# Kernel optimization log

Hardware: AMD Instinct MI355X
Metric: run time of the kernel (lower is better)

## Reference

```python
import jax, jax.numpy as jnp
import numpy as np

NUM_NODES = 10000


def setup_inputs() -> dict:
    key = jax.random.key(0)
    k1, k2, k3, k4 = jax.random.split(key, 4)
    x = jax.random.normal(k1, (NUM_NODES, 128), dtype=jnp.float32)
    edge_index = jax.random.randint(k2, (2, 640000), 0, NUM_NODES, dtype=jnp.int64)
    W = jax.random.normal(k3, (128, 128), dtype=jnp.float32) * (1.0 / np.sqrt(128))
    b = jax.random.normal(k4, (128,), dtype=jnp.float32) * 0.01
    return {"x": x, "edge_index": edge_index, "W": W, "b": b}


def reference(x, edge_index, W, b):
    src, dst = edge_index[0], edge_index[1]
    num_nodes = x.shape[0]
    # scatter-add: aggregated[dst] += x[src]
    aggregated = jax.ops.segment_sum(x[src], dst, num_segments=num_nodes)
    # in-degree normalization (clamped at 1)
    degree = jax.ops.segment_sum(jnp.ones_like(dst, dtype=x.dtype), dst,
                                 num_segments=num_nodes)
    degree = jnp.maximum(degree, 1.0)
    aggregated = aggregated / degree[:, None]
    # linear (y = h @ W.T + b) + ReLU
    out = jax.nn.relu(jnp.einsum('nd,od->no', aggregated + x, W) + b)
    return out
```

## Files before the change

### kernel.cpp

```cpp
#include <hip/hip_runtime.h>
#include <hip/hip_bf16.h>
#include <hip/hip_fp8.h>
#include <hip/hip_cooperative_groups.h>

namespace cg = cooperative_groups;

#define NB    64
#define EPB   10000
#define NPAD  10240
#define NPT   40
#define NGEMM 625
#define LCAP  1024
#define GRID_FUSED (NGEMM + NB)
#define SMEM_BYTES 40496

typedef __bf16 bf16_8 __attribute__((ext_vector_type(8)));
typedef float f32_2 __attribute__((ext_vector_type(2)));
typedef float f32_4 __attribute__((ext_vector_type(4)));
typedef float f32_8 __attribute__((ext_vector_type(8)));

__device__ __forceinline__ void gemm_role(unsigned char* smem, int bx,
    const float* __restrict__ x, const float* __restrict__ W,
    __hip_bfloat16* __restrict__ zb, unsigned char* __restrict__ zb8) {
  float* ctile = (float*)smem;
  const int rowbase = bx * 16;
  const int wid = threadIdx.x >> 6;
  const int lane = threadIdx.x & 63;
  const int m16 = lane & 15;
  const int quad = lane >> 4;

  union { bf16_8 v; __hip_bfloat16 h8[8]; } ac[4];
  const float* arow = x + (size_t)(rowbase + m16) * 128 + quad * 8;
#pragma unroll
  for (int kk = 0; kk < 4; ++kk) {
    f32_8 af = *(const f32_8*)(arow + kk * 32);
#pragma unroll
    for (int j = 0; j < 8; ++j) ac[kk].h8[j] = __float2bfloat16(af[j]);
  }
#pragma unroll
  for (int ct = 0; ct < 2; ++ct) {
    int colbase = wid * 32 + ct * 16;
    const float* brow = W + (size_t)(colbase + m16) * 128 + quad * 8;
    f32_4 c = {0.f, 0.f, 0.f, 0.f};
#pragma unroll
    for (int kk = 0; kk < 4; ++kk) {
      f32_8 bf = *(const f32_8*)(brow + kk * 32);
      union { bf16_8 v; __hip_bfloat16 h8[8]; } bc;
#pragma unroll
      for (int j = 0; j < 8; ++j) bc.h8[j] = __float2bfloat16(bf[j]);
      c = __builtin_amdgcn_mfma_f32_16x16x32_bf16(ac[kk].v, bc.v, c, 0, 0, 0);
    }
#pragma unroll
    for (int r = 0; r < 4; ++r)
      ctile[(quad * 4 + r) * 132 + colbase + m16] = c[r];
  }
  __syncthreads();

  const int row = threadIdx.x >> 4;
  const int cs = (threadIdx.x & 15) * 8;
  const float* src = ctile + row * 132 + cs;
  f32_4 a0 = *(const f32_4*)(src);
  f32_4 a1 = *(const f32_4*)(src + 4);
  union { uint4 u; __hip_bfloat16 h[8]; } hb;
  union { uint2 u; unsigned char c[8]; } q8;
#pragma unroll
  for (int j = 0; j < 4; ++j) {
    hb.h[j] = __float2bfloat16(a0[j]);
    hb.h[4 + j] = __float2bfloat16(a1[j]);
    q8.c[j] = __hip_fp8_e4m3(a0[j]).__x;
    q8.c[4 + j] = __hip_fp8_e4m3(a1[j]).__x;
  }
  *(uint4*)(zb + (size_t)(rowbase + row) * 128 + cs) = hb.u;
  *(uint2*)(zb8 + (size_t)(rowbase + row) * 128 + cs) = q8.u;
}

__device__ __forceinline__ void sort_role(unsigned char* smem, int b,
    const int* __restrict__ ei, int E,
    unsigned short* __restrict__ bins, unsigned int* __restrict__ combo) {
  int* h = (int*)smem;
  unsigned short* sorted = (unsigned short*)(smem + 20480);
  int* wsum = (int*)(smem + 40480);

  const int t = threadIdx.x;
  const int4* src4 = (const int4*)(ei) + b * (EPB / 4);
  const int4* dst4 = (const int4*)(ei + E) + b * (EPB / 4);

  for (int i = t; i < NPAD / 2; i += 256) h[i] = 0;
  __syncthreads();

  for (int i = t; i < EPB / 4; i += 256) {
    int4 d = dst4[i];
    atomicAdd(&h[d.x >> 1], 1 << ((d.x & 1) * 16));
    atomicAdd(&h[d.y >> 1], 1 << ((d.y & 1) * 16));
    atomicAdd(&h[d.z >> 1], 1 << ((d.z & 1) * 16));
    atomicAdd(&h[d.w >> 1], 1 << ((d.w & 1) * 16));
  }
  __syncthreads();

  int raw[NPT];
  const int lo = t * NPT;
  int sum = 0;
#pragma unroll
  for (int j = 0; j < NPT; j += 2) {
    int pair = h[(lo + j) >> 1];
    raw[j] = pair & 0xFFFF;
    raw[j + 1] = (pair >> 16) & 0xFFFF;
    sum += raw[j] + raw[j + 1];
  }
  int incl = sum;
#pragma unroll
  for (int off = 1; off < 64; off <<= 1) {
    int v = __shfl_up(incl, off);
    if ((t & 63) >= off) incl += v;
  }
  if ((t & 63) == 63) wsum[t >> 6] = incl;
  __syncthreads();
  int wb = 0;
  for (int w = 0; w < (t >> 6); ++w) wb += wsum[w];
  int run = wb + incl - sum;

  unsigned int cpack[NPT];
#pragma unroll
  for (int j = 0; j < NPT; j += 2) {
    int r0 = run; run += raw[j];
    int r1 = run; run += raw[j + 1];
    h[(lo + j) >> 1] = (r1 << 16) | r0;
    cpack[j]     = ((unsigned)raw[j] << 16) | (unsigned)r0;
    cpack[j + 1] = ((unsigned)raw[j + 1] << 16) | (unsigned)r1;
  }
  __syncthreads();

  unsigned int* crow = combo + (size_t)b * NPAD + lo;
#pragma unroll
  for (int j = 0; j < NPT; j += 4)
    *(uint4*)(crow + j) = make_uint4(cpack[j], cpack[j+1], cpack[j+2], cpack[j+3]);

  for (int i = t; i < EPB / 4; i += 256) {
    int4 s4 = src4[i];
    int4 d4 = dst4[i];
    int ss[4] = {s4.x, s4.y, s4.z, s4.w};
    int dd[4] = {d4.x, d4.y, d4.z, d4.w};
#pragma unroll
    for (int u = 0; u < 4; ++u) {
      int nn = dd[u];
      int sh = (nn & 1) * 16;
      int pos = (atomicAdd(&h[nn >> 1], 1 << sh) >> sh) & 0xFFFF;
      sorted[pos] = (unsigned short)ss[u];
    }
  }
  __syncthreads();

  unsigned int* outb = (unsigned int*)(bins + (size_t)b * EPB);
  const unsigned int* s32 = (const unsigned int*)sorted;
  for (int i = t; i < EPB / 2; i += 256) outb[i] = s32[i];
}

__device__ __forceinline__ void agg_quad(unsigned char* smem, int q,
    const unsigned int* __restrict__ combo, const unsigned short* __restrict__ bins,
    const unsigned char* __restrict__ zb8, const __hip_bfloat16* __restrict__ zb,
    const float* __restrict__ bias, float* __restrict__ out, int N) {
  unsigned int* trans = (unsigned int*)smem;
  unsigned short* list = (unsigned short*)(smem + 1024);
  int* cursor = (int*)(smem + 9216);

  const int t = threadIdx.x;
  const int wid = t >> 6;
  const int lane = t & 63;
  const int n0 = q * 4;

  __syncthreads();
  if (t < 4) cursor[t] = 0;
  if (t < 64) {
    uint4 cm = *(const uint4*)(combo + (size_t)t * NPAD + n0);
    trans[t] = cm.x; trans[64 + t] = cm.y; trans[128 + t] = cm.z; trans[192 + t] = cm.w;
  }
  __syncthreads();

  const int n = n0 + wid;
  unsigned int cc = trans[wid * 64 + lane];
  int c = (int)(cc >> 16);
  int o = (int)(cc & 0xFFFF);

  int p = atomicAdd(&cursor[wid], c);

  {
    const unsigned short* bk = bins + (size_t)lane * EPB + o;
    unsigned short* L = list + wid * LCAP;
    unsigned short s0 = 0, s1 = 0, s2 = 0;
    if (c > 0) s0 = bk[0];
    if (c > 1) s1 = bk[1];
    if (c > 2) s2 = bk[2];
    if (c > 0 && p < LCAP) L[p] = s0;
    if (c > 1 && p + 1 < LCAP) L[p + 1] = s1;
    if (c > 2 && p + 2 < LCAP) L[p + 2] = s2;
    for (int j = 3; j < c; ++j)
      if (p + j < LCAP) L[p + j] = bk[j];
  }
  __syncthreads();

  const int m = cursor[wid];
  const int g = lane >> 3;
  const int sub = lane & 7;
  int mm = m < LCAP ? m : LCAP;
  const unsigned short* L = list + wid * LCAP;
  const unsigned char* z8base = zb8 + sub * 16;

  float acc[16];
#pragma unroll
  for (int k = 0; k < 16; ++k) acc[k] = 0.f;

  for (int e = 0; e < mm; e += 64) {
    uint4 v[8];
#pragma unroll
    for (int u = 0; u < 8; ++u) {
      int idx = e + u * 8 + g;
      v[u] = make_uint4(0u, 0u, 0u, 0u);
      if (idx < mm) {
        int s = L[idx];
        v[u] = *(const uint4*)(z8base + (size_t)s * 128);
      }
    }
#pragma unroll
    for (int u = 0; u < 8; ++u) {
      f32_2 p01 = __builtin_amdgcn_cvt_pk_f32_fp8((int)v[u].x, false);
      f32_2 p23 = __builtin_amdgcn_cvt_pk_f32_fp8((int)v[u].x, true);
      f32_2 p45 = __builtin_amdgcn_cvt_pk_f32_fp8((int)v[u].y, false);
      f32_2 p67 = __builtin_amdgcn_cvt_pk_f32_fp8((int)v[u].y, true);
      f32_2 p89 = __builtin_amdgcn_cvt_pk_f32_fp8((int)v[u].z, false);
      f32_2 pab = __builtin_amdgcn_cvt_pk_f32_fp8((int)v[u].z, true);
      f32_2 pcd = __builtin_amdgcn_cvt_pk_f32_fp8((int)v[u].w, false);
      f32_2 pef = __builtin_amdgcn_cvt_pk_f32_fp8((int)v[u].w, true);
      acc[0] += p01[0];  acc[1] += p01[1];  acc[2] += p23[0];  acc[3] += p23[1];
      acc[4] += p45[0];  acc[5] += p45[1];  acc[6] += p67[0];  acc[7] += p67[1];
      acc[8] += p89[0];  acc[9] += p89[1];  acc[10] += pab[0]; acc[11] += pab[1];
      acc[12] += pcd[0]; acc[13] += pcd[1]; acc[14] += pef[0]; acc[15] += pef[1];
    }
  }
#pragma unroll
  for (int k = 0; k < 16; ++k) {
    acc[k] += __shfl_xor(acc[k], 8);
    acc[k] += __shfl_xor(acc[k], 16);
    acc[k] += __shfl_xor(acc[k], 32);
  }

  if (g == 0 && n < N) {
    float inv = 1.f / (float)(m > 0 ? m : 1);
    const __hip_bfloat16* znp = zb + (size_t)n * 128 + sub * 16;
    bf16_8 z0 = *(const bf16_8*)znp;
    bf16_8 z1 = *(const bf16_8*)(znp + 8);
    const float* bp = bias + sub * 16;
    f32_8 b0 = *(const f32_8*)bp;
    f32_8 b1 = *(const f32_8*)(bp + 8);
    float r[16];
#pragma unroll
    for (int k = 0; k < 8; ++k) {
      float v2 = acc[k] * inv + (float)z0[k] + b0[k];
      r[k] = v2 > 0.f ? v2 : 0.f;
    }
#pragma unroll
    for (int k = 0; k < 8; ++k) {
      float v2 = acc[8 + k] * inv + (float)z1[k] + b1[k];
      r[8 + k] = v2 > 0.f ? v2 : 0.f;
    }
    float* o2 = out + (size_t)n * 128 + sub * 16;
    *(float4*)(o2)      = make_float4(r[0], r[1], r[2], r[3]);
    *(float4*)(o2 + 4)  = make_float4(r[4], r[5], r[6], r[7]);
    *(float4*)(o2 + 8)  = make_float4(r[8], r[9], r[10], r[11]);
    *(float4*)(o2 + 12) = make_float4(r[12], r[13], r[14], r[15]);
  }
}

__global__ void __launch_bounds__(256, 3) k_all(
    const float* __restrict__ x, const int* __restrict__ ei,
    const float* __restrict__ W, const float* __restrict__ bias,
    __hip_bfloat16* __restrict__ zb, unsigned char* __restrict__ zb8,
    unsigned short* __restrict__ bins, unsigned int* __restrict__ combo,
    float* __restrict__ out, int E, int N) {
  __shared__ __align__(16) unsigned char smem[SMEM_BYTES];
  if (blockIdx.x < NGEMM) gemm_role(smem, blockIdx.x, x, W, zb, zb8);
  else sort_role(smem, blockIdx.x - NGEMM, ei, E, bins, combo);
  __threadfence();
  cg::this_grid().sync();
  const int NQ = N >> 2;
  for (int q = blockIdx.x; q < NQ; q += gridDim.x)
    agg_quad(smem, q, combo, bins, zb8, zb, bias, out, N);
}

__global__ void __launch_bounds__(256, 3) k_phase1(
    const float* __restrict__ x, const int* __restrict__ ei,
    const float* __restrict__ W,
    __hip_bfloat16* __restrict__ zb, unsigned char* __restrict__ zb8,
    unsigned short* __restrict__ bins, unsigned int* __restrict__ combo, int E) {
  __shared__ __align__(16) unsigned char smem[SMEM_BYTES];
  if (blockIdx.x < NGEMM) gemm_role(smem, blockIdx.x, x, W, zb, zb8);
  else sort_role(smem, blockIdx.x - NGEMM, ei, E, bins, combo);
}

__global__ void __launch_bounds__(256) k_phase2(
    const unsigned int* __restrict__ combo, const unsigned short* __restrict__ bins,
    const unsigned char* __restrict__ zb8, const __hip_bfloat16* __restrict__ zb,
    const float* __restrict__ bias, float* __restrict__ out, int N) {
  __shared__ __align__(16) unsigned char smem[9232];
  agg_quad(smem, blockIdx.x, combo, bins, zb8, zb, bias, out, N);
}

extern "C" void kernel_launch(void* const* d_in, const int* in_sizes, int n_in,
                              void* d_out, int out_size, void* d_ws, size_t ws_size,
                              hipStream_t stream) {
  const float* x = (const float*)d_in[0];
  const int* ei = (const int*)d_in[1];
  const float* W = (const float*)d_in[2];
  const float* b = (const float*)d_in[3];
  float* out = (float*)d_out;

  const int N = in_sizes[0] / 128;
  const int E = in_sizes[1] / 2;

  char* ws = (char*)d_ws;
  size_t off = 0;
  auto carve = [&](size_t bytes) {
    void* p = ws + off;
    off = (off + bytes + 255) & ~(size_t)255;
    return p;
  };
  __hip_bfloat16* zb = (__hip_bfloat16*)carve((size_t)N * 128 * 2);
  unsigned char* zb8 = (unsigned char*)carve((size_t)N * 128);
  unsigned short* bins = (unsigned short*)carve((size_t)NB * EPB * 2);
  unsigned int* combo = (unsigned int*)carve((size_t)NB * NPAD * 4);

  static int coop = -1;
  bool done = false;
  if (coop != 0) {
    bool try_now = true;
    if (coop == -1) {
      hipStreamCaptureStatus st = hipStreamCaptureStatusNone;
      (void)hipStreamIsCapturing(stream, &st);
      if (st != hipStreamCaptureStatusNone) try_now = false;
    }
    if (try_now) {
      void* args[] = {(void*)&x, (void*)&ei, (void*)&W, (void*)&b,
                      (void*)&zb, (void*)&zb8, (void*)&bins, (void*)&combo,
                      (void*)&out, (void*)&E, (void*)&N};
      hipError_t err = hipLaunchCooperativeKernel((const void*)k_all, dim3(GRID_FUSED),
                                                  dim3(256), args, 0, stream);
      if (err == hipSuccess) {
        coop = 1;
        done = true;
      } else {
        coop = 0;
        (void)hipGetLastError();
      }
    }
  }
  if (!done) {
    k_phase1<<<GRID_FUSED, 256, 0, stream>>>(x, ei, W, zb, zb8, bins, combo, E);
    k_phase2<<<N / 4, 256, 0, stream>>>(combo, bins, zb8, zb, b, out, N);
  }
}
```

Baseline: 101.0 us.

## Replace cooperative grid-sync kernel with two launches and wave-scan list building

Drops the cooperative single-kernel path with a grid-wide barrier and always launches a phase-1 kernel followed by a separate aggregation kernel with 2500 blocks and higher occupancy bounds. The aggregation kernel replaces the shared-memory atomic cursor with a wavefront shuffle prefix scan, which removes a block barrier. The sort role's edge loops are manually unrolled to issue two int4 loads per iteration for more memory parallelism. The cost is an extra kernel launch boundary in exchange for avoiding grid-sync overhead and the persistent-loop imbalance.

```diff
diff --git a/kernel.cpp b/kernel.cpp
--- a/kernel.cpp
+++ b/kernel.cpp
@@ -1,9 +1,6 @@
 #include <hip/hip_runtime.h>
 #include <hip/hip_bf16.h>
 #include <hip/hip_fp8.h>
-#include <hip/hip_cooperative_groups.h>
-
-namespace cg = cooperative_groups;
 
 #define NB    64
 #define EPB   10000
@@ -11,7 +8,6 @@
 #define NPT   40
 #define NGEMM 625
 #define LCAP  1024
-#define GRID_FUSED (NGEMM + NB)
 #define SMEM_BYTES 40496
 
 typedef __bf16 bf16_8 __attribute__((ext_vector_type(8)));
@@ -88,8 +84,29 @@
   for (int i = t; i < NPAD / 2; i += 256) h[i] = 0;
   __syncthreads();
 
-  for (int i = t; i < EPB / 4; i += 256) {
-    int4 d = dst4[i];
+#pragma unroll
+  for (int k = 0; k < 4; ++k) {
+    int i0 = t + k * 512;
+    int4 d0 = dst4[i0];
+    int4 d1 = dst4[i0 + 256];
+    atomicAdd(&h[d0.x >> 1], 1 << ((d0.x & 1) * 16));
+    atomicAdd(&h[d0.y >> 1], 1 << ((d0.y & 1) * 16));
+    atomicAdd(&h[d0.z >> 1], 1 << ((d0.z & 1) * 16));
+    atomicAdd(&h[d0.w >> 1], 1 << ((d0.w & 1) * 16));
+    atomicAdd(&h[d1.x >> 1], 1 << ((d1.x & 1) * 16));
+    atomicAdd(&h[d1.y >> 1], 1 << ((d1.y & 1) * 16));
+    atomicAdd(&h[d1.z >> 1], 1 << ((d1.z & 1) * 16));
+    atomicAdd(&h[d1.w >> 1], 1 << ((d1.w & 1) * 16));
+  }
+  {
+    int4 d = dst4[2048 + t];
+    atomicAdd(&h[d.x >> 1], 1 << ((d.x & 1) * 16));
+    atomicAdd(&h[d.y >> 1], 1 << ((d.y & 1) * 16));
+    atomicAdd(&h[d.z >> 1], 1 << ((d.z & 1) * 16));
+    atomicAdd(&h[d.w >> 1], 1 << ((d.w & 1) * 16));
+  }
+  if (t < 196) {
+    int4 d = dst4[2304 + t];
     atomicAdd(&h[d.x >> 1], 1 << ((d.x & 1) * 16));
     atomicAdd(&h[d.y >> 1], 1 << ((d.y & 1) * 16));
     atomicAdd(&h[d.z >> 1], 1 << ((d.z & 1) * 16));
@@ -135,11 +152,28 @@
   for (int j = 0; j < NPT; j += 4)
     *(uint4*)(crow + j) = make_uint4(cpack[j], cpack[j+1], cpack[j+2], cpack[j+3]);
 
-  for (int i = t; i < EPB / 4; i += 256) {
-    int4 s4 = src4[i];
-    int4 d4 = dst4[i];
-    int ss[4] = {s4.x, s4.y, s4.z, s4.w};
-    int dd[4] = {d4.x, d4.y, d4.z, d4.w};
+#pragma unroll
+  for (int k = 0; k < 4; ++k) {
+    int i0 = t + k * 512;
+    int4 s0 = src4[i0];
+    int4 d0 = dst4[i0];
+    int4 s1 = src4[i0 + 256];
+    int4 d1 = dst4[i0 + 256];
+    int ss[8] = {s0.x, s0.y, s0.z, s0.w, s1.x, s1.y, s1.z, s1.w};
+    int dd[8] = {d0.x, d0.y, d0.z, d0.w, d1.x, d1.y, d1.z, d1.w};
+#pragma unroll
+    for (int u = 0; u < 8; ++u) {
+      int nn = dd[u];
+      int sh = (nn & 1) * 16;
+      int pos = (atomicAdd(&h[nn >> 1], 1 << sh) >> sh) & 0xFFFF;
+      sorted[pos] = (unsigned short)ss[u];
+    }
+  }
+  {
+    int4 s = src4[2048 + t];
+    int4 d = dst4[2048 + t];
+    int ss[4] = {s.x, s.y, s.z, s.w};
+    int dd[4] = {d.x, d.y, d.z, d.w};
 #pragma unroll
     for (int u = 0; u < 4; ++u) {
       int nn = dd[u];
@@ -148,6 +182,19 @@
       sorted[pos] = (unsigned short)ss[u];
     }
   }
+  if (t < 196) {
+    int4 s = src4[2304 + t];
+    int4 d = dst4[2304 + t];
+    int ss[4] = {s.x, s.y, s.z, s.w};
+    int dd[4] = {d.x, d.y, d.z, d.w};
+#pragma unroll
+    for (int u = 0; u < 4; ++u) {
+      int nn = dd[u];
+      int sh = (nn & 1) * 16;
+      int pos = (atomicAdd(&h[nn >> 1], 1 << sh) >> sh) & 0xFFFF;
+      sorted[pos] = (unsigned short)ss[u];
+    }
+  }
   __syncthreads();
 
   unsigned int* outb = (unsigned int*)(bins + (size_t)b * EPB);
@@ -155,37 +202,51 @@
   for (int i = t; i < EPB / 2; i += 256) outb[i] = s32[i];
 }
 
-__device__ __forceinline__ void agg_quad(unsigned char* smem, int q,
+__global__ void __launch_bounds__(256) k_phase1(
+    const float* __restrict__ x, const int* __restrict__ ei,
+    const float* __restrict__ W,
+    __hip_bfloat16* __restrict__ zb, unsigned char* __restrict__ zb8,
+    unsigned short* __restrict__ bins, unsigned int* __restrict__ combo, int E) {
+  __shared__ __align__(16) unsigned char smem[SMEM_BYTES];
+  if (blockIdx.x < NGEMM) gemm_role(smem, blockIdx.x, x, W, zb, zb8);
+  else sort_role(smem, blockIdx.x - NGEMM, ei, E, bins, combo);
+}
+
+__global__ void __launch_bounds__(256, 6) k_agg(
     const unsigned int* __restrict__ combo, const unsigned short* __restrict__ bins,
     const unsigned char* __restrict__ zb8, const __hip_bfloat16* __restrict__ zb,
     const float* __restrict__ bias, float* __restrict__ out, int N) {
-  unsigned int* trans = (unsigned int*)smem;
-  unsigned short* list = (unsigned short*)(smem + 1024);
-  int* cursor = (int*)(smem + 9216);
+  __shared__ unsigned int trans[4][64];
+  __shared__ unsigned short list[4][LCAP];
 
   const int t = threadIdx.x;
   const int wid = t >> 6;
   const int lane = t & 63;
-  const int n0 = q * 4;
-
-  __syncthreads();
-  if (t < 4) cursor[t] = 0;
+  const int n0 = blockIdx.x * 4;
+
   if (t < 64) {
     uint4 cm = *(const uint4*)(combo + (size_t)t * NPAD + n0);
-    trans[t] = cm.x; trans[64 + t] = cm.y; trans[128 + t] = cm.z; trans[192 + t] = cm.w;
+    trans[0][t] = cm.x; trans[1][t] = cm.y; trans[2][t] = cm.z; trans[3][t] = cm.w;
   }
   __syncthreads();
 
   const int n = n0 + wid;
-  unsigned int cc = trans[wid * 64 + lane];
+  unsigned int cc = trans[wid][lane];
   int c = (int)(cc >> 16);
   int o = (int)(cc & 0xFFFF);
 
-  int p = atomicAdd(&cursor[wid], c);
+  int incl = c;
+#pragma unroll
+  for (int off = 1; off < 64; off <<= 1) {
+    int v = __shfl_up(incl, off);
+    if (lane >= off) incl += v;
+  }
+  const int m = __shfl(incl, 63);
+  int p = incl - c;
 
   {
     const unsigned short* bk = bins + (size_t)lane * EPB + o;
-    unsigned short* L = list + wid * LCAP;
+    unsigned short* L = list[wid];
     unsigned short s0 = 0, s1 = 0, s2 = 0;
     if (c > 0) s0 = bk[0];
     if (c > 1) s1 = bk[1];
@@ -196,13 +257,11 @@
     for (int j = 3; j < c; ++j)
       if (p + j < LCAP) L[p + j] = bk[j];
   }
-  __syncthreads();
-
-  const int m = cursor[wid];
+
   const int g = lane >> 3;
   const int sub = lane & 7;
   int mm = m < LCAP ? m : LCAP;
-  const unsigned short* L = list + wid * LCAP;
+  const unsigned short* L = list[wid];
   const unsigned char* z8base = zb8 + sub * 16;
 
   float acc[16];
@@ -270,40 +329,6 @@
   }
 }
 
-__global__ void __launch_bounds__(256, 3) k_all(
-    const float* __restrict__ x, const int* __restrict__ ei,
-    const float* __restrict__ W, const float* __restrict__ bias,
-    __hip_bfloat16* __restrict__ zb, unsigned char* __restrict__ zb8,
-    unsigned short* __restrict__ bins, unsigned int* __restrict__ combo,
-    float* __restrict__ out, int E, int N) {
-  __shared__ __align__(16) unsigned char smem[SMEM_BYTES];
-  if (blockIdx.x < NGEMM) gemm_role(smem, blockIdx.x, x, W, zb, zb8);
-  else sort_role(smem, blockIdx.x - NGEMM, ei, E, bins, combo);
-  __threadfence();
-  cg::this_grid().sync();
-  const int NQ = N >> 2;
-  for (int q = blockIdx.x; q < NQ; q += gridDim.x)
-    agg_quad(smem, q, combo, bins, zb8, zb, bias, out, N);
-}
-
-__global__ void __launch_bounds__(256, 3) k_phase1(
-    const float* __restrict__ x, const int* __restrict__ ei,
-    const float* __restrict__ W,
-    __hip_bfloat16* __restrict__ zb, unsigned char* __restrict__ zb8,
-    unsigned short* __restrict__ bins, unsigned int* __restrict__ combo, int E) {
-  __shared__ __align__(16) unsigned char smem[SMEM_BYTES];
-  if (blockIdx.x < NGEMM) gemm_role(smem, blockIdx.x, x, W, zb, zb8);
-  else sort_role(smem, blockIdx.x - NGEMM, ei, E, bins, combo);
-}
-
-__global__ void __launch_bounds__(256) k_phase2(
-    const unsigned int* __restrict__ combo, const unsigned short* __restrict__ bins,
-    const unsigned char* __restrict__ zb8, const __hip_bfloat16* __restrict__ zb,
-    const float* __restrict__ bias, float* __restrict__ out, int N) {
-  __shared__ __align__(16) unsigned char smem[9232];
-  agg_quad(smem, blockIdx.x, combo, bins, zb8, zb, bias, out, N);
-}
-
 extern "C" void kernel_launch(void* const* d_in, const int* in_sizes, int n_in,
                               void* d_out, int out_size, void* d_ws, size_t ws_size,
                               hipStream_t stream) {
@@ -328,32 +353,6 @@
   unsigned short* bins = (unsigned short*)carve((size_t)NB * EPB * 2);
   unsigned int* combo = (unsigned int*)carve((size_t)NB * NPAD * 4);
 
-  static int coop = -1;
-  bool done = false;
-  if (coop != 0) {
-    bool try_now = true;
-    if (coop == -1) {
-      hipStreamCaptureStatus st = hipStreamCaptureStatusNone;
-      (void)hipStreamIsCapturing(stream, &st);
-      if (st != hipStreamCaptureStatusNone) try_now = false;
-    }
-    if (try_now) {
-      void* args[] = {(void*)&x, (void*)&ei, (void*)&W, (void*)&b,
-                      (void*)&zb, (void*)&zb8, (void*)&bins, (void*)&combo,
-                      (void*)&out, (void*)&E, (void*)&N};
-      hipError_t err = hipLaunchCooperativeKernel((const void*)k_all, dim3(GRID_FUSED),
-                                                  dim3(256), args, 0, stream);
-      if (err == hipSuccess) {
-        coop = 1;
-        done = true;
-      } else {
-        coop = 0;
-        (void)hipGetLastError();
-      }
-    }
-  }
-  if (!done) {
-    k_phase1<<<GRID_FUSED, 256, 0, stream>>>(x, ei, W, zb, zb8, bins, combo, E);
-    k_phase2<<<N / 4, 256, 0, stream>>>(combo, bins, zb8, zb, b, out, N);
-  }
-}
+  k_phase1<<<NGEMM + NB, 256, 0, stream>>>(x, ei, W, zb, zb8, bins, combo, E);
+  k_agg<<<N / 4, 256, 0, stream>>>(combo, bins, zb8, zb, b, out, N);
+}
```

New measurement: 183.8 us. +82.0%, slower.
